# Performance work log

Measured on AMD Instinct MI355X. Metric: run time of the kernel, lower is better.

Reference implementation:

```python
import jax, jax.numpy as jnp
import numpy as np
from jax import lax

B, S, IN, H, HEAD, OUT = 256, 512, 64, 1024, 128, 64


def setup_inputs() -> dict:
    key = jax.random.key(0)
    ks = jax.random.split(key, 9)
    sc = 0.05
    return {
        "x": jax.random.normal(ks[0], (B, S, IN), jnp.float32),
        "W_ih": jax.random.normal(ks[1], (4 * H, IN), jnp.float32) * sc,
        "b_ih": jax.random.normal(ks[2], (4 * H,), jnp.float32) * sc,
        "W_hh": jax.random.normal(ks[3], (4 * H, H), jnp.float32) * sc,
        "b_hh": jax.random.normal(ks[4], (4 * H,), jnp.float32) * sc,
        "W_dense": jax.random.normal(ks[5], (HEAD, H), jnp.float32) * sc,
        "b_dense": jax.random.normal(ks[6], (HEAD,), jnp.float32) * sc,
        "W_dense2": jax.random.normal(ks[7], (OUT, HEAD), jnp.float32) * sc,
        "b_dense2": jax.random.normal(ks[8], (OUT,), jnp.float32) * sc,
    }


def reference(x, W_ih, b_ih, W_hh, b_hh, W_dense, b_dense, W_dense2, b_dense2):
    batch = x.shape[0]
    hid = W_hh.shape[1]
    # Precompute input-to-gate projections for all timesteps in one big GEMM.
    # x: [B,S,IN] -> xg: [S,B,4H]
    xg = jnp.einsum("bsi,gi->sbg", x, W_ih) + b_ih + b_hh

    def step(carry, xg_t):
        h, c = carry
        gates = xg_t + h @ W_hh.T  # [B,4H]; PyTorch LSTMCell gate order i,f,g,o
        i, f, g, o = jnp.split(gates, 4, axis=-1)
        c = jax.nn.sigmoid(f) * c + jax.nn.sigmoid(i) * jnp.tanh(g)
        h = jax.nn.sigmoid(o) * jnp.tanh(c)
        pred = jax.nn.relu(h @ W_dense.T + b_dense) @ W_dense2.T + b_dense2
        return (h, c), pred

    h0 = jnp.zeros((batch, hid), x.dtype)
    c0 = jnp.zeros((batch, hid), x.dtype)
    _, out = lax.scan(step, (h0, c0), xg)  # out: [S,B,OUT]
    return jnp.swapaxes(out, 0, 1)  # [B,S,OUT]
```

## Files before the change

kernel.cpp:

```cpp
#include <hip/hip_runtime.h>

typedef _Float16 half_t;
typedef _Float16 half8 __attribute__((ext_vector_type(8)));
typedef _Float16 half4 __attribute__((ext_vector_type(4)));
typedef float float4v __attribute__((ext_vector_type(4)));

#define BB    256
#define SS    512
#define IND   64
#define HH    1024
#define HEADD 128
#define OUTD  64
#define NKT   34
#define WLDS_HALVES (4 * NKT * 512)
#define PRE_STRIDE 68
#define DP_OFF   (WLDS_HALVES * 2 + 4 * 16 * PRE_STRIDE * 4)
#define FLAG_OFF (DP_OFF + 3 * 64 * 4 * 4)
#define SMEM_BYTES (FLAG_OFF + 32)
#define BUFV (BB * HH)
#define DCNT_OFF 10240
#define SYNC_WORDS 10368

#define MFMA16(a, b, acc) __builtin_amdgcn_mfma_f32_16x16x32_f16(a, b, acc, 0, 0, 0)

__device__ half_t g_hA[(size_t)(SS + 1) * BUFV];
__device__ half_t g_dbuf[(size_t)SS * 256 * HEADD];
__device__ unsigned int g_sync[SYNC_WORDS];

__device__ __forceinline__ void astore8(half_t* p, half4 v) {
  union { half4 h; unsigned long long u; } r; r.h = v;
  __hip_atomic_store((unsigned long long*)p, r.u, __ATOMIC_RELAXED,
                     __HIP_MEMORY_SCOPE_AGENT);
}
__device__ __forceinline__ void astore2(half_t* p, half_t v) {
  union { half_t h; unsigned short u; } r; r.h = v;
  __hip_atomic_store((unsigned short*)p, r.u, __ATOMIC_RELAXED,
                     __HIP_MEMORY_SCOPE_AGENT);
}


__global__ __launch_bounds__(256) void init_state() {
  const size_t i = (size_t)blockIdx.x * 256 + threadIdx.x;
  *(unsigned long long*)(g_hA + i * 4) = 0ULL;
  if (blockIdx.x == 0)
    for (int j = threadIdx.x; j < SYNC_WORDS; j += 256) g_sync[j] = 0;
}

__global__ __launch_bounds__(256) void pack_x(const float* __restrict__ x,
                                              half_t* __restrict__ xA) {
  const int t = blockIdx.x, mt = blockIdx.y;
  const int tid = threadIdx.x;
  const int kt = tid >> 7;
  const int lane = (tid >> 1) & 63;
  const int jh = (tid & 1) * 4;
  const int row = mt * 16 + (lane & 15);
  const int k = kt * 32 + (lane >> 4) * 8 + jh;
  const float* s = x + (size_t)row * SS * IND + (size_t)t * IND + k;
  half_t* d = xA + (((size_t)t * 16 + mt) * 2 + kt) * 512 + lane * 8 + jh;
  d[0] = (half_t)s[0]; d[1] = (half_t)s[1];
  d[2] = (half_t)s[2]; d[3] = (half_t)s[3];
}

__global__ __launch_bounds__(256) void frag_pack(const float* __restrict__ src,
                                                 half_t* __restrict__ dst, int K) {
  const int cb = blockIdx.x;
  const int tid = threadIdx.x;
  const int lane = tid & 63;
  const int u = tid >> 6;
  const int nkt = K >> 5;
  const int row = cb * 16 + (lane & 15);
  for (int kt = u; kt < nkt; kt += 4) {
    const int k = kt * 32 + (lane >> 4) * 8;
    const float* s = src + (size_t)row * K + k;
    half8 h;
    #pragma unroll
    for (int j = 0; j < 8; ++j) h[j] = (half_t)s[j];
    *(half8*)(dst + ((size_t)cb * nkt + kt) * 512 + lane * 8) = h;
  }
}

__global__ __launch_bounds__(512, 2) void lstm_persistent(
    const float* __restrict__ W_hh, const float* __restrict__ W_ih,
    const float* __restrict__ b_ih, const float* __restrict__ b_hh,
    const half_t* __restrict__ xA, const half_t* __restrict__ Wd_f,
    const float* __restrict__ bd, const half_t* __restrict__ Wd2_f,
    const float* __restrict__ bd2, float* __restrict__ out) {
  extern __shared__ char smem[];
  half_t* Wlds = (half_t*)smem;
  float* pre = (float*)(smem + (size_t)WLDS_HALVES * 2);
  float* dp = (float*)(smem + DP_OFF);
  unsigned* flg = (unsigned*)(smem + FLAG_OFF);

  const int bid = blockIdx.x;
  const int xcd = bid & 7;
  const int mtile = xcd >> 1;
  const int jtile = ((bid >> 3) << 1) | (xcd & 1);
  const int j0 = jtile * 16;
  const int tid = threadIdx.x;
  const int wave = tid >> 6;
  const int lane = tid & 63;
  const int rn = lane & 15;
  const int kq = lane >> 4;

  {
    const int g = wave & 3;
    const int row = g * HH + j0 + rn;
    for (int kt = (wave >> 2); kt < NKT; kt += 2) {
      const int k = kt * 32 + kq * 8;
      const float* s = (k < HH) ? (W_hh + (size_t)row * HH + k)
                                : (W_ih + (size_t)row * IND + (k - HH));
      half8 hv;
      #pragma unroll
      for (int j = 0; j < 8; ++j) hv[j] = (half_t)s[j];
      *(half8*)(Wlds + ((size_t)g * NKT + kt) * 512 + lane * 8) = hv;
    }
  }
  if (tid < 8) flg[tid] = 0;
  __syncthreads();

  unsigned short* slotp =
      (unsigned short*)(g_sync + ((size_t)(mtile * 64 + jtile)) * 32);
  const unsigned long long* pollp =
      (const unsigned long long*)(g_sync + ((size_t)(mtile * 64 + lane)) * 32);
  unsigned int* dcnt = g_sync + DCNT_OFF + mtile * 32;

  if (wave < 4) {
    const int crow = lane >> 2;
    const int hl = (lane & 3) * 4;
    float bsum[4][4];
    #pragma unroll
    for (int g = 0; g < 4; ++g) {
      const float4v bi = *(const float4v*)(b_ih + g * HH + j0 + hl);
      const float4v bh = *(const float4v*)(b_hh + g * HH + j0 + hl);
      #pragma unroll
      for (int j = 0; j < 4; ++j) bsum[g][j] = bi[j] + bh[j];
    }
    float4v creg = {0.f, 0.f, 0.f, 0.f};

    const int mtA = mtile * 4 + wave;
    float* pw = pre + wave * (16 * PRE_STRIDE);

    const int col_s = j0 + hl;
    const int ktw = col_s >> 5;
    const int kqw = (col_s & 31) >> 3;
    const int jw = col_s & 7;
    const size_t hoff =
        (((size_t)(mtA * 32 + ktw)) * 64 + kqw * 16 + crow) * 8 + jw;

    const half_t* habase = g_hA + ((size_t)mtA * 32) * 512 + lane * 8;
    const half_t* bp = Wlds + lane * 8;
    unsigned short* myslot = slotp + wave;

    half8 breg0[8], breg1[8], breg2[8], breg3[8];
    #pragma unroll
    for (int kt = 0; kt < 8; ++kt) {
      breg0[kt] = *(const half8*)(bp + (size_t)(0 * NKT + kt) * 512);
      breg1[kt] = *(const half8*)(bp + (size_t)(1 * NKT + kt) * 512);
      breg2[kt] = *(const half8*)(bp + (size_t)(2 * NKT + kt) * 512);
      breg3[kt] = *(const half8*)(bp + (size_t)(3 * NKT + kt) * 512);
    }

    for (int t = 0; t < SS; ++t) {
      float4v a0 = {0.f, 0.f, 0.f, 0.f}, a1 = {0.f, 0.f, 0.f, 0.f};
      float4v a2 = {0.f, 0.f, 0.f, 0.f}, a3 = {0.f, 0.f, 0.f, 0.f};

      const half_t* xp = xA + (((size_t)t * 16 + mtA) * 2) * 512 + lane * 8;
      {
        const half8 xv0 = *(const half8*)xp;
        const half8 xv1 = *(const half8*)(xp + 512);
        a0 = MFMA16(xv0, *(const half8*)(bp + (size_t)(0 * NKT + 32) * 512), a0);
        a1 = MFMA16(xv0, *(const half8*)(bp + (size_t)(1 * NKT + 32) * 512), a1);
        a2 = MFMA16(xv0, *(const half8*)(bp + (size_t)(2 * NKT + 32) * 512), a2);
        a3 = MFMA16(xv0, *(const half8*)(bp + (size_t)(3 * NKT + 32) * 512), a3);
        a0 = MFMA16(xv1, *(const half8*)(bp + (size_t)(0 * NKT + 33) * 512), a0);
        a1 = MFMA16(xv1, *(const half8*)(bp + (size_t)(1 * NKT + 33) * 512), a1);
        a2 = MFMA16(xv1, *(const half8*)(bp + (size_t)(2 * NKT + 33) * 512), a2);
        a3 = MFMA16(xv1, *(const half8*)(bp + (size_t)(3 * NKT + 33) * 512), a3);
      }

      if (t >= 1) {
        const unsigned tt = (unsigned)t;
        if (wave == 0) {
          for (;;) {
            const unsigned long long v = __hip_atomic_load(
                pollp, __ATOMIC_RELAXED, __HIP_MEMORY_SCOPE_AGENT);
            const unsigned f0 = (unsigned)(v & 0xffffu);
            const unsigned f1 = (unsigned)((v >> 16) & 0xffffu);
            const unsigned f2 = (unsigned)((v >> 32) & 0xffffu);
            const unsigned f3 = (unsigned)(v >> 48);
            if (__all((int)(f0 >= tt && f1 >= tt && f2 >= tt && f3 >= tt)))
              break;
            __builtin_amdgcn_s_sleep(1);
          }
          asm volatile("" ::: "memory");
          if (lane == 0)
            __hip_atomic_store(&flg[3], tt, __ATOMIC_RELEASE,
                               __HIP_MEMORY_SCOPE_WORKGROUP);
        } else {
          while (__hip_atomic_load(&flg[3], __ATOMIC_ACQUIRE,
                                   __HIP_MEMORY_SCOPE_WORKGROUP) < tt)
            __builtin_amdgcn_s_sleep(1);
        }
        asm volatile("" ::: "memory");
      }

      const half_t* ap = habase + (size_t)t * BUFV;
      #pragma unroll
      for (int kt = 0; kt < 8; ++kt) {
        const half8 av = *(const half8*)(ap + (size_t)kt * 512);
        a0 = MFMA16(av, breg0[kt], a0);
        a1 = MFMA16(av, breg1[kt], a1);
        a2 = MFMA16(av, breg2[kt], a2);
        a3 = MFMA16(av, breg3[kt], a3);
      }
      #pragma unroll 8
      for (int kt = 8; kt < 32; ++kt) {
        const half8 av = *(const half8*)(ap + (size_t)kt * 512);
        a0 = MFMA16(av, *(const half8*)(bp + (size_t)(0 * NKT + kt) * 512), a0);
        a1 = MFMA16(av, *(const half8*)(bp + (size_t)(1 * NKT + kt) * 512), a1);
        a2 = MFMA16(av, *(const half8*)(bp + (size_t)(2 * NKT + kt) * 512), a2);
        a3 = MFMA16(av, *(const half8*)(bp + (size_t)(3 * NKT + kt) * 512), a3);
      }

      #pragma unroll
      for (int r = 0; r < 4; ++r) {
        const int rl = (kq * 4 + r) * PRE_STRIDE;
        pw[rl + rn] = a0[r];
        pw[rl + 16 + rn] = a1[r];
        pw[rl + 32 + rn] = a2[r];
        pw[rl + 48 + rn] = a3[r];
      }

      const float4v pg0 = *(const float4v*)(pw + crow * PRE_STRIDE + hl);
      const float4v pg1 = *(const float4v*)(pw + crow * PRE_STRIDE + 16 + hl);
      const float4v pg2 = *(const float4v*)(pw + crow * PRE_STRIDE + 32 + hl);
      const float4v pg3 = *(const float4v*)(pw + crow * PRE_STRIDE + 48 + hl);
      half4 hnew;
      #pragma unroll
      for (int jj = 0; jj < 4; ++jj) {
        const float ig = pg0[jj] + bsum[0][jj];
        const float fg = pg1[jj] + bsum[1][jj];
        const float gg = pg2[jj] + bsum[2][jj];
        const float og = pg3[jj] + bsum[3][jj];
        const float is = 1.f / (1.f + __expf(-ig));
        const float fs = 1.f / (1.f + __expf(-fg));
        const float os = 1.f / (1.f + __expf(-og));
        const float gt = tanhf(gg);
        const float cn = fs * creg[jj] + is * gt;
        creg[jj] = cn;
        hnew[jj] = (half_t)(os * tanhf(cn));
      }
      astore8(g_hA + (size_t)(t + 1) * BUFV + hoff, hnew);

      __builtin_amdgcn_s_waitcnt(0);
      if (lane == 0)
        __hip_atomic_store(myslot, (unsigned short)(t + 1), __ATOMIC_RELAXED,
                           __HIP_MEMORY_SCOPE_AGENT);
    }

    if (wave == 0) {
      const unsigned tt = (unsigned)SS;
      for (;;) {
        const unsigned long long v = __hip_atomic_load(
            pollp, __ATOMIC_RELAXED, __HIP_MEMORY_SCOPE_AGENT);
        const unsigned f0 = (unsigned)(v & 0xffffu);
        const unsigned f1 = (unsigned)((v >> 16) & 0xffffu);
        const unsigned f2 = (unsigned)((v >> 32) & 0xffffu);
        const unsigned f3 = (unsigned)(v >> 48);
        if (__all((int)(f0 >= tt && f1 >= tt && f2 >= tt && f3 >= tt))) break;
        __builtin_amdgcn_s_sleep(1);
      }
      asm volatile("" ::: "memory");
      if (lane == 0)
        __hip_atomic_store(&flg[3], tt, __ATOMIC_RELEASE,
                           __HIP_MEMORY_SCOPE_WORKGROUP);
    }

  } else if (jtile < 32) {
    const int u = wave - 4;
    const int rb = jtile >> 3, cb = jtile & 7;
    const int mt = mtile * 4 + rb;
    const half_t* hb = g_hA + ((size_t)mt * 32 + u * 8) * 512 + lane * 8;
    const half_t* bb = Wd_f + ((size_t)cb * 32 + u * 8) * 512 + lane * 8;

    half8 bbreg[8];
    #pragma unroll
    for (int kt = 0; kt < 8; ++kt)
      bbreg[kt] = *(const half8*)(bb + (size_t)kt * 512);

    for (int s = 1; s <= SS; ++s) {
      while (__hip_atomic_load(&flg[3], __ATOMIC_ACQUIRE,
                               __HIP_MEMORY_SCOPE_WORKGROUP) < (unsigned)s)
        __builtin_amdgcn_s_sleep(2);
      asm volatile("" ::: "memory");

      const half_t* ap = hb + (size_t)s * BUFV;
      float4v acc = {0.f, 0.f, 0.f, 0.f};
      #pragma unroll
      for (int kt = 0; kt < 8; ++kt)
        acc = MFMA16(*(const half8*)(ap + (size_t)kt * 512), bbreg[kt], acc);

      if (u) {
        if (s > 1)
          while (__hip_atomic_load(&flg[4], __ATOMIC_ACQUIRE,
                                   __HIP_MEMORY_SCOPE_WORKGROUP) <
                 (unsigned)(s - 1))
            __builtin_amdgcn_s_sleep(1);
        *(float4v*)(dp + ((size_t)(u - 1) * 64 + lane) * 4) = acc;
        __hip_atomic_store(&flg[u - 1], (unsigned)s, __ATOMIC_RELEASE,
                           __HIP_MEMORY_SCOPE_WORKGROUP);
      } else {
        for (;;) {
          const unsigned f0 = __hip_atomic_load(&flg[0], __ATOMIC_ACQUIRE,
                                                __HIP_MEMORY_SCOPE_WORKGROUP);
          const unsigned f1 = __hip_atomic_load(&flg[1], __ATOMIC_ACQUIRE,
                                                __HIP_MEMORY_SCOPE_WORKGROUP);
          const unsigned f2 = __hip_atomic_load(&flg[2], __ATOMIC_ACQUIRE,
                                                __HIP_MEMORY_SCOPE_WORKGROUP);
          if (f0 >= (unsigned)s && f1 >= (unsigned)s && f2 >= (unsigned)s) break;
          __builtin_amdgcn_s_sleep(1);
        }
        asm volatile("" ::: "memory");
        #pragma unroll
        for (int i = 0; i < 3; ++i) {
          const float4v p = *(const float4v*)(dp + ((size_t)i * 64 + lane) * 4);
          #pragma unroll
          for (int r = 0; r < 4; ++r) acc[r] += p[r];
        }
        __hip_atomic_store(&flg[4], (unsigned)s, __ATOMIC_RELEASE,
                           __HIP_MEMORY_SCOPE_WORKGROUP);
        const int dcol = cb * 16 + rn;
        const float bv = bd[dcol];
        half_t* db = g_dbuf + (((size_t)(s - 1) * 16 + mt) * 16) * HEADD + dcol;
        #pragma unroll
        for (int r = 0; r < 4; ++r)
          astore2(db + (size_t)(kq * 4 + r) * HEADD,
                  (half_t)fmaxf(acc[r] + bv, 0.f));
        __builtin_amdgcn_s_waitcnt(0);
        if (lane == 0)
          __hip_atomic_fetch_add(dcnt, 1u, __ATOMIC_RELAXED,
                                 __HIP_MEMORY_SCOPE_AGENT);
      }
    }

  } else if (jtile < 48 && wave == 4) {
    const int task = jtile - 32;
    const int rb = task >> 2, cb2 = task & 3;
    const int mt = mtile * 4 + rb;
    const int m0 = mtile * 64;
    const half_t* bp2 = Wd2_f + (size_t)cb2 * 4 * 512 + lane * 8;
    half8 b2reg[4];
    #pragma unroll
    for (int kt = 0; kt < 4; ++kt)
      b2reg[kt] = *(const half8*)(bp2 + (size_t)kt * 512);
    for (int d = 0; d < SS; ++d) {
      if (lane == 0) {
        const unsigned tgt = 32u * (unsigned)(d + 1);
        while (__hip_atomic_load(dcnt, __ATOMIC_RELAXED,
                                 __HIP_MEMORY_SCOPE_AGENT) < tgt)
          __builtin_amdgcn_s_sleep(16);
      }
      asm volatile("" ::: "memory");
      const half_t* ap = g_dbuf + (((size_t)d * 16 + mt) * 16) * HEADD;
      float4v acc = {0.f, 0.f, 0.f, 0.f};
      #pragma unroll
      for (int kt = 0; kt < 4; ++kt) {
        const half8 af =
            *(const half8*)(ap + (size_t)rn * HEADD + kt * 32 + kq * 8);
        acc = MFMA16(af, b2reg[kt], acc);
      }
      const int ocol = cb2 * 16 + rn;
      const float bv = bd2[ocol];
      #pragma unroll
      for (int r = 0; r < 4; ++r) {
        const int row = m0 + rb * 16 + kq * 4 + r;
        out[(size_t)row * (SS * OUTD) + (size_t)d * OUTD + ocol] = acc[r] + bv;
      }
    }
  }
}

extern "C" void kernel_launch(void* const* d_in, const int* in_sizes, int n_in,
                              void* d_out, int out_size, void* d_ws, size_t ws_size,
                              hipStream_t stream) {
  const float* x        = (const float*)d_in[0];
  const float* W_ih     = (const float*)d_in[1];
  const float* b_ih     = (const float*)d_in[2];
  const float* W_hh     = (const float*)d_in[3];
  const float* b_hh     = (const float*)d_in[4];
  const float* W_dense  = (const float*)d_in[5];
  const float* b_dense  = (const float*)d_in[6];
  const float* W_dense2 = (const float*)d_in[7];
  const float* b_dense2 = (const float*)d_in[8];
  float* out = (float*)d_out;

  char* p = (char*)d_ws;
  half_t* xA    = (half_t*)p; p += (size_t)SS * 16 * 1024 * 2;
  half_t* Wd_f  = (half_t*)p; p += (size_t)8 * 32 * 512 * 2;
  half_t* Wd2_f = (half_t*)p; p += (size_t)4 * 4 * 512 * 2;

  init_state<<<256, 256, 0, stream>>>();
  pack_x<<<dim3(SS, 16), 256, 0, stream>>>(x, xA);
  frag_pack<<<HEADD / 16, 256, 0, stream>>>(W_dense, Wd_f, HH);
  frag_pack<<<OUTD / 16, 256, 0, stream>>>(W_dense2, Wd2_f, HEADD);

  hipFuncSetAttribute((const void*)lstm_persistent,
                      hipFuncAttributeMaxDynamicSharedMemorySize, SMEM_BYTES);
  void* args[] = {(void*)&W_hh, (void*)&W_ih, (void*)&b_ih, (void*)&b_hh,
                  (void*)&xA, (void*)&Wd_f, (void*)&b_dense,
                  (void*)&Wd2_f, (void*)&b_dense2, (void*)&out};
  hipLaunchCooperativeKernel((void*)lstm_persistent, dim3(256), dim3(512),
                             args, SMEM_BYTES, stream);
}
```

Baseline: 4.431 ms.

## Replace per-wave slot polling with per-workgroup aggregated atomic counter barrier

The per-wave 16-bit progress slots, which the poller read as 64-bit words across 64 lanes, are replaced by a single global counter per mtile. Each workgroup first counts its four waves in an LDS counter, and the last wave issues one agent-scope fetch_add. Waiters spin on that counter without s_sleep, and wave 0 snapshots the counter early so the first check overlaps the x-projection MFMAs. The aim is to lower the latency and memory traffic of the per-timestep cross-workgroup barrier, at the cost of atomic contention on one hot counter.

```diff
diff --git a/kernel.cpp b/kernel.cpp
--- a/kernel.cpp
+++ b/kernel.cpp
@@ -16,8 +16,9 @@
 #define PRE_STRIDE 68
 #define DP_OFF   (WLDS_HALVES * 2 + 4 * 16 * PRE_STRIDE * 4)
 #define FLAG_OFF (DP_OFF + 3 * 64 * 4 * 4)
-#define SMEM_BYTES (FLAG_OFF + 32)
+#define SMEM_BYTES (FLAG_OFF + 96)
 #define BUFV (BB * HH)
+#define CNT_OFF  8192
 #define DCNT_OFF 10240
 #define SYNC_WORDS 10368
 
@@ -90,6 +91,7 @@
   float* pre = (float*)(smem + (size_t)WLDS_HALVES * 2);
   float* dp = (float*)(smem + DP_OFF);
   unsigned* flg = (unsigned*)(smem + FLAG_OFF);
+  unsigned* wgdone = flg + 8;
 
   const int bid = blockIdx.x;
   const int xcd = bid & 7;
@@ -116,12 +118,10 @@
     }
   }
   if (tid < 8) flg[tid] = 0;
+  if (tid >= 8 && tid < 24) wgdone[tid - 8] = 0;
   __syncthreads();
 
-  unsigned short* slotp =
-      (unsigned short*)(g_sync + ((size_t)(mtile * 64 + jtile)) * 32);
-  const unsigned long long* pollp =
-      (const unsigned long long*)(g_sync + ((size_t)(mtile * 64 + lane)) * 32);
+  unsigned int* cnt = g_sync + CNT_OFF + mtile * 32;
   unsigned int* dcnt = g_sync + DCNT_OFF + mtile * 32;
 
   if (wave < 4) {
@@ -149,7 +149,6 @@
 
     const half_t* habase = g_hA + ((size_t)mtA * 32) * 512 + lane * 8;
     const half_t* bp = Wlds + lane * 8;
-    unsigned short* myslot = slotp + wave;
 
     half8 breg0[8], breg1[8], breg2[8], breg3[8];
     #pragma unroll
@@ -161,6 +160,11 @@
     }
 
     for (int t = 0; t < SS; ++t) {
+      unsigned csnap = 0;
+      if (t >= 1 && wave == 0)
+        csnap = __hip_atomic_load(cnt, __ATOMIC_RELAXED,
+                                  __HIP_MEMORY_SCOPE_AGENT);
+
       float4v a0 = {0.f, 0.f, 0.f, 0.f}, a1 = {0.f, 0.f, 0.f, 0.f};
       float4v a2 = {0.f, 0.f, 0.f, 0.f}, a3 = {0.f, 0.f, 0.f, 0.f};
 
@@ -181,25 +185,18 @@
       if (t >= 1) {
         const unsigned tt = (unsigned)t;
         if (wave == 0) {
-          for (;;) {
-            const unsigned long long v = __hip_atomic_load(
-                pollp, __ATOMIC_RELAXED, __HIP_MEMORY_SCOPE_AGENT);
-            const unsigned f0 = (unsigned)(v & 0xffffu);
-            const unsigned f1 = (unsigned)((v >> 16) & 0xffffu);
-            const unsigned f2 = (unsigned)((v >> 32) & 0xffffu);
-            const unsigned f3 = (unsigned)(v >> 48);
-            if (__all((int)(f0 >= tt && f1 >= tt && f2 >= tt && f3 >= tt)))
-              break;
-            __builtin_amdgcn_s_sleep(1);
-          }
+          const unsigned tgt = 64u * tt;
+          unsigned v = csnap;
+          while (v < tgt)
+            v = __hip_atomic_load(cnt, __ATOMIC_RELAXED,
+                                  __HIP_MEMORY_SCOPE_AGENT);
           asm volatile("" ::: "memory");
           if (lane == 0)
             __hip_atomic_store(&flg[3], tt, __ATOMIC_RELEASE,
                                __HIP_MEMORY_SCOPE_WORKGROUP);
         } else {
           while (__hip_atomic_load(&flg[3], __ATOMIC_ACQUIRE,
-                                   __HIP_MEMORY_SCOPE_WORKGROUP) < tt)
-            __builtin_amdgcn_s_sleep(1);
+                                   __HIP_MEMORY_SCOPE_WORKGROUP) < tt) {}
         }
         asm volatile("" ::: "memory");
       }
@@ -253,26 +250,23 @@
       astore8(g_hA + (size_t)(t + 1) * BUFV + hoff, hnew);
 
       __builtin_amdgcn_s_waitcnt(0);
-      if (lane == 0)
-        __hip_atomic_store(myslot, (unsigned short)(t + 1), __ATOMIC_RELAXED,
-                           __HIP_MEMORY_SCOPE_AGENT);
+      if (lane == 0) {
+        const unsigned old = atomicAdd(&wgdone[t & 15], 1u);
+        if (old == 3u) {
+          wgdone[t & 15] = 0u;
+          __hip_atomic_fetch_add(cnt, 1u, __ATOMIC_RELAXED,
+                                 __HIP_MEMORY_SCOPE_AGENT);
+        }
+      }
     }
 
     if (wave == 0) {
-      const unsigned tt = (unsigned)SS;
-      for (;;) {
-        const unsigned long long v = __hip_atomic_load(
-            pollp, __ATOMIC_RELAXED, __HIP_MEMORY_SCOPE_AGENT);
-        const unsigned f0 = (unsigned)(v & 0xffffu);
-        const unsigned f1 = (unsigned)((v >> 16) & 0xffffu);
-        const unsigned f2 = (unsigned)((v >> 32) & 0xffffu);
-        const unsigned f3 = (unsigned)(v >> 48);
-        if (__all((int)(f0 >= tt && f1 >= tt && f2 >= tt && f3 >= tt))) break;
+      while (__hip_atomic_load(cnt, __ATOMIC_RELAXED,
+                               __HIP_MEMORY_SCOPE_AGENT) < 64u * (unsigned)SS)
         __builtin_amdgcn_s_sleep(1);
-      }
       asm volatile("" ::: "memory");
       if (lane == 0)
-        __hip_atomic_store(&flg[3], tt, __ATOMIC_RELEASE,
+        __hip_atomic_store(&flg[3], (unsigned)SS, __ATOMIC_RELEASE,
                            __HIP_MEMORY_SCOPE_WORKGROUP);
     }
 
```

Measured after the change: 5.504 ms. 1.24x slower.
